# Optimization experiments

Measured on AMD Instinct MI355X. Metric: run time of the kernel, lower is better.

## Reference

```python
import jax, jax.numpy as jnp
import numpy as np

K = 3          # spline order
NUM = 32       # grid intervals G
IN_DIM = 256
OUT_DIM = 512
BATCH = 2048


def _b_spline_basis(x, grid, k):
    """Cox-de-Boor recursion. x: (B, I); grid: (I, G+2k+1) -> (B, I, G+k)."""
    xg = x[:, :, None]                      # (B, I, 1)
    g = grid[None, :, :]                    # (1, I, G+2k+1)
    val = ((xg >= g[:, :, :-1]) & (xg < g[:, :, 1:])).astype(x.dtype)
    for p in range(1, k + 1):
        left = (xg - g[:, :, :-(p + 1)]) / (g[:, :, p:-1] - g[:, :, :-(p + 1)])
        right = (g[:, :, p + 1:] - xg) / (g[:, :, p + 1:] - g[:, :, 1:-p])
        val = left * val[:, :, :-1] + right * val[:, :, 1:]
    return val                               # (B, I, G+k)


def setup_inputs() -> dict:
    key = jax.random.key(0)
    k1, k2, k3 = jax.random.split(key, 3)
    x = jax.random.normal(k1, (BATCH, IN_DIM), dtype=jnp.float32)
    # uniform grid on [-1, 1], extended by k knots on each side (extend_grid)
    base = np.linspace(-1.0, 1.0, NUM + 1)
    h = 2.0 / NUM
    ext = np.concatenate([base[0] - h * np.arange(K, 0, -1), base,
                          base[-1] + h * np.arange(1, K + 1)]).astype(np.float32)
    grid = jnp.tile(jnp.asarray(ext)[None, :], (IN_DIM, 1))  # (I, G+2k+1)
    coef = 0.1 * jax.random.normal(k2, (IN_DIM, OUT_DIM, NUM + K), dtype=jnp.float32)
    scale_base = jax.random.normal(k3, (IN_DIM, OUT_DIM), dtype=jnp.float32) / np.sqrt(IN_DIM).astype(np.float32)
    scale_sp = jnp.ones((IN_DIM, OUT_DIM), dtype=jnp.float32) / np.sqrt(IN_DIM).astype(np.float32)
    mask = jnp.ones((IN_DIM, OUT_DIM), dtype=jnp.float32)
    return {"x": x, "grid": grid, "coef": coef,
            "scale_base": scale_base, "scale_sp": scale_sp, "mask": mask}


def reference(x, grid, coef, scale_base, scale_sp, mask):
    base = jax.nn.silu(x)                                   # b(x) residual, (B, I)
    bases = _b_spline_basis(x, grid, K)                     # (B, I, G+k)
    # coef2curve: einsum('ijk,jlk->ijl') in pykan -> (B, I, O)
    y = jnp.einsum('bik,iok->bio', bases, coef)
    y = scale_base[None, :, :] * base[:, :, None] + scale_sp[None, :, :] * y
    y = mask[None, :, :] * y
    return jnp.sum(y, axis=1)                               # (B, O)
```

## Files before the change

kernel.cpp:

```cpp
#include <hip/hip_runtime.h>
#include <math.h>

#define BATCH   2048
#define IN_DIM  256
#define OUT_DIM 512
#define NK      35
#define KS      48
#define KG      6
#define BTILE   128
#define OTILE   128
#define ICHUNK  32
#define NSPLIT  8
#define NBUF    4
#define COEFS_BYTES ((size_t)IN_DIM * OUT_DIM * KS * 2)
#define PART_ELEMS  ((size_t)BATCH * OUT_DIM)

__device__ __forceinline__ unsigned short f2bf(float x) {
    unsigned u = __float_as_uint(x);
    u += 0x7FFF + ((u >> 16) & 1);
    return (unsigned short)(u >> 16);
}
__device__ __forceinline__ float bf2f(unsigned short h) {
    return __uint_as_float(((unsigned)h) << 16);
}
__device__ __forceinline__ unsigned pack2(unsigned short a, unsigned short b) {
    return (unsigned)a | ((unsigned)b << 16);
}

typedef __bf16 bf16x8 __attribute__((ext_vector_type(8)));
typedef float  f32x16 __attribute__((ext_vector_type(16)));
typedef int    i32x4  __attribute__((ext_vector_type(4)));
typedef unsigned int u32;

__device__ __forceinline__ void gload_lds16(const void* g, void* l) {
    __builtin_amdgcn_global_load_lds((const __attribute__((address_space(1))) u32*)g,
                                     (__attribute__((address_space(3))) u32*)l, 16, 0, 0);
}

__device__ __forceinline__ unsigned lds_off(const void* p) {
    return (unsigned)(uintptr_t)(const __attribute__((address_space(3))) char*)p;
}

__device__ __forceinline__ i32x4 ds_read128(unsigned base, int off) {
    i32x4 r;
    asm volatile("ds_read_b128 %0, %1 offset:%c2"
                 : "=v"(r) : "v"(base), "i"(off));
    return r;
}
__device__ __forceinline__ bf16x8 as_bf16x8(i32x4 v) {
    bf16x8 r; __builtin_memcpy(&r, &v, 16); return r;
}

#define PR 32
__global__ __launch_bounds__(256) void kan_prep(
    const float* __restrict__ coef,
    const float* __restrict__ scale_base,
    const float* __restrict__ scale_sp,
    const float* __restrict__ mask,
    unsigned short* __restrict__ coefS)
{
    __shared__ float sc[PR * NK];
    __shared__ float sspm[PR], ssbm[PR];
    const int t    = threadIdx.x;
    const int row0 = blockIdx.x * PR;

    {
        const float4* csrc = (const float4*)(coef + (size_t)row0 * NK);
        float4* cdst = (float4*)sc;
        cdst[t] = csrc[t];
        if (t < 24) cdst[t + 256] = csrc[t + 256];
    }
    if (t < PR) {
        float m = mask[row0 + t];
        sspm[t] = scale_sp[row0 + t] * m;
        ssbm[t] = scale_base[row0 + t] * m;
    }
    __syncthreads();

    if (t < PR * 6) {
        int r = t / 6;
        int q = t - r * 6;
        float spm = sspm[r];
        const float* c = sc + r * NK;
        uint4 v = make_uint4(0u, 0u, 0u, 0u);
        if (q < 4) {
            const float* cq = c + q * 8;
            v.x = pack2(f2bf(cq[0] * spm), f2bf(cq[1] * spm));
            v.y = pack2(f2bf(cq[2] * spm), f2bf(cq[3] * spm));
            v.z = pack2(f2bf(cq[4] * spm), f2bf(cq[5] * spm));
            v.w = pack2(f2bf(cq[6] * spm), f2bf(cq[7] * spm));
        } else if (q == 4) {
            float sbm = ssbm[r];
            unsigned short hi = f2bf(sbm);
            unsigned short lo = f2bf(sbm - bf2f(hi));
            v.x = pack2(f2bf(c[32] * spm), f2bf(c[33] * spm));
            v.y = pack2(f2bf(c[34] * spm), 0);
            v.z = pack2(hi, hi);
            v.w = pack2(lo, 0);
        }
        int g = row0 + r;
        size_t di = ((size_t)(((g >> 9) * 4 + ((g >> 7) & 3)) * 6 + q)) * 128
                  + (size_t)(g & 127);
        ((uint4*)coefS)[di] = v;
    }
}

__global__ __launch_bounds__(256, 2) void kan_mfma(
    const float* __restrict__ x,
    const unsigned short* __restrict__ coefS,
    float* __restrict__ part)
{
    __shared__ __align__(16) short sA[2 * BTILE * KS];
    __shared__ __align__(16) short sB[NBUF * OTILE * KS];

    const int t    = threadIdx.x;
    const int w    = t >> 6;
    const int lane = t & 63;
    const int l31  = lane & 31, lh = lane >> 5;
    const int wr   = w & 1;
    const int wc   = w >> 1;
    const int o0   = blockIdx.x * OTILE;
    const int b0   = blockIdx.y * BTILE;
    const int ic0  = blockIdx.z * ICHUNK;
    const bool bTh = (t >= 128);
    const int wbase = t & 64;

    {
        uint4 z = make_uint4(0, 0, 0, 0);
        #pragma unroll
        for (int u = 0; u < 6; ++u) {
            int idx = t + 256 * u;
            if (idx < (2 * BTILE * KS * 2) / 16) ((uint4*)sA)[idx] = z;
        }
    }

    f32x16 acc00 = {}, acc01 = {}, acc10 = {}, acc11 = {};

    float xreg = 0.0f;
    int ojb0 = 0, ojb1 = 0;

    auto stageA = [&](short* abuf, int row, float xv, int& ojbn) {
        #pragma unroll
        for (int qq = 0; qq < 4; ++qq) {
            int k = ojbn + qq;
            abuf[((k >> 3) * BTILE + row) * 8 + (k & 7)] = 0;
        }
        float xn = (xv + 1.1875f) * 16.0f;
        float jf = floorf(xn);
        int   j  = (int)jf;
        float u  = xn - jf;
        bool valid = (xn >= 0.0f) && (j <= 37);
        float u2 = u * u, u3 = u2 * u;
        float w0 = (1.0f / 6.0f) * (1.0f - 3.0f * u + 3.0f * u2 - u3);
        float w1 = (1.0f / 6.0f) * (3.0f * u3 - 6.0f * u2 + 4.0f);
        float w2 = (1.0f / 6.0f) * (-3.0f * u3 + 3.0f * u2 + 3.0f * u + 1.0f);
        float w3 = (1.0f / 6.0f) * u3;
        int jb = j - 3;
        if (valid) {
            if ((unsigned)jb < 35u) {
                int k = jb;     abuf[((k >> 3) * BTILE + row) * 8 + (k & 7)] = f2bf(w0);
            }
            if ((unsigned)(jb + 1) < 35u) {
                int k = jb + 1; abuf[((k >> 3) * BTILE + row) * 8 + (k & 7)] = f2bf(w1);
            }
            if ((unsigned)(jb + 2) < 35u) {
                int k = jb + 2; abuf[((k >> 3) * BTILE + row) * 8 + (k & 7)] = f2bf(w2);
            }
            if ((unsigned)(jb + 3) < 35u) {
                int k = jb + 3; abuf[((k >> 3) * BTILE + row) * 8 + (k & 7)] = f2bf(w3);
            }
        }
        ojbn = min(max(jb, 0), 31);
        float sig = 1.0f / (1.0f + __expf(-xv));
        float s   = xv * sig;
        unsigned short shi = f2bf(s);
        unsigned short slo = f2bf(s - bf2f(shi));
        short* k4 = abuf + (4 * BTILE + row) * 8;
        *(unsigned int*)(k4 + 4) = pack2(shi, slo);
        k4[6] = shi;
    };

    auto issueB = [&](int i, int buf) {
        const char* gsrc = (const char*)coefS
                         + ((size_t)i * 4 + (o0 >> 7)) * (KG * OTILE * 8 * 2);
        #pragma unroll
        for (int q = 0; q < 6; ++q) {
            int slot = wbase + (t & 63) + 128 * q;
            gload_lds16(gsrc + slot * 16,
                        (void*)(sB + buf * (OTILE * KS) + (wbase + 128 * q) * 8));
        }
    };

    __syncthreads();

    if (!bTh) {
        float x0 = x[(size_t)(b0 + t) * IN_DIM + ic0];
        stageA(sA, t, x0, ojb0);
        xreg = x[(size_t)(b0 + t) * IN_DIM + ic0 + 1];
    } else {
        issueB(ic0,     0);
        issueB(ic0 + 1, 1);
        issueB(ic0 + 2, 2);
    }
    if (bTh) asm volatile("s_waitcnt vmcnt(12)" ::: "memory");
    else     asm volatile("s_waitcnt lgkmcnt(0)" ::: "memory");
    __builtin_amdgcn_s_barrier();
    __builtin_amdgcn_sched_barrier(0);

    const unsigned sAoff = lds_off(sA);
    const unsigned sBoff = lds_off(sB);

    auto body = [&](int it, int& ojbn) {
        if (bTh && it + 1 < ICHUNK) {
            int ip3 = (it + 3 < ICHUNK) ? (it + 3) : (ICHUNK - 1);
            issueB(ic0 + ip3, (it + 3) & (NBUF - 1));
        }

        const int cur = it & 1;
        const unsigned Abo = sAoff
            + (unsigned)(cur * (BTILE * KS) + (lh * BTILE + wr * 64 + l31) * 8) * 2u;
        const unsigned Bbo = sBoff
            + (unsigned)((it & (NBUF - 1)) * (OTILE * KS)
                         + (lh * OTILE + wc * 64 + l31) * 8) * 2u;

        i32x4 a0r[3], a1r[3], b0r[3], b1r[3];
        #pragma unroll
        for (int s = 0; s < 3; ++s) {
            a0r[s] = ds_read128(Abo, s * 4096);
            a1r[s] = ds_read128(Abo, s * 4096 + 512);
            b0r[s] = ds_read128(Bbo, s * 4096);
            b1r[s] = ds_read128(Bbo, s * 4096 + 512);
        }
        asm volatile("s_waitcnt lgkmcnt(0)" ::: "memory");
        __builtin_amdgcn_sched_barrier(0);

        __builtin_amdgcn_s_setprio(1);
        #pragma unroll
        for (int s = 0; s < 3; ++s) {
            acc00 = __builtin_amdgcn_mfma_f32_32x32x16_bf16(as_bf16x8(a0r[s]), as_bf16x8(b0r[s]), acc00, 0, 0, 0);
            acc01 = __builtin_amdgcn_mfma_f32_32x32x16_bf16(as_bf16x8(a0r[s]), as_bf16x8(b1r[s]), acc01, 0, 0, 0);
            acc10 = __builtin_amdgcn_mfma_f32_32x32x16_bf16(as_bf16x8(a1r[s]), as_bf16x8(b0r[s]), acc10, 0, 0, 0);
            acc11 = __builtin_amdgcn_mfma_f32_32x32x16_bf16(as_bf16x8(a1r[s]), as_bf16x8(b1r[s]), acc11, 0, 0, 0);
        }
        __builtin_amdgcn_s_setprio(0);

        if (!bTh && it + 1 < ICHUNK) {
            stageA(sA + (cur ^ 1) * (BTILE * KS), t, xreg, ojbn);
            if (it + 2 < ICHUNK)
                xreg = x[(size_t)(b0 + t) * IN_DIM + ic0 + it + 2];
        }

        if (it + 1 < ICHUNK) {
            if (bTh) asm volatile("s_waitcnt vmcnt(12)" ::: "memory");
            else     asm volatile("s_waitcnt lgkmcnt(0)" ::: "memory");
            __builtin_amdgcn_s_barrier();
            __builtin_amdgcn_sched_barrier(0);
        }
    };

    for (int itp = 0; itp < ICHUNK / 2; ++itp) {
        body(2 * itp,     ojb1);
        body(2 * itp + 1, ojb0);
    }

    __syncthreads();

    float* tp = (float*)sA + w * (32 * 36);
    float* pdst = part + (size_t)blockIdx.z * PART_ELEMS;
    #pragma unroll
    for (int r = 0; r < 2; ++r) {
        #pragma unroll
        for (int c = 0; c < 2; ++c) {
            const f32x16& acc = (r == 0) ? ((c == 0) ? acc00 : acc01)
                                         : ((c == 0) ? acc10 : acc11);
            #pragma unroll
            for (int reg = 0; reg < 16; ++reg) {
                int row = (reg & 3) + 8 * (reg >> 2) + 4 * lh;
                tp[row * 36 + l31] = acc[reg];
            }
            int cc = (lane & 7) * 4;
            #pragma unroll
            for (int j = 0; j < 4; ++j) {
                int rr = j * 8 + (lane >> 3);
                float4 v = *(float4*)&tp[rr * 36 + cc];
                int rowg = b0 + wr * 64 + r * 32 + rr;
                int colg = o0 + wc * 64 + c * 32 + cc;
                *(float4*)&pdst[(size_t)rowg * OUT_DIM + colg] = v;
            }
        }
    }
}

__global__ __launch_bounds__(256) void kan_reduce(
    const float4* __restrict__ part, float4* __restrict__ out)
{
    const size_t e = (size_t)blockIdx.x * 256 + threadIdx.x;
    float4 s = part[e];
    #pragma unroll
    for (int z = 1; z < NSPLIT; ++z) {
        float4 v = part[(size_t)z * (PART_ELEMS / 4) + e];
        s.x += v.x; s.y += v.y; s.z += v.z; s.w += v.w;
    }
    out[e] = s;
}

extern "C" void kernel_launch(void* const* d_in, const int* in_sizes, int n_in,
                              void* d_out, int out_size, void* d_ws, size_t ws_size,
                              hipStream_t stream) {
    const float* x          = (const float*)d_in[0];
    const float* coef       = (const float*)d_in[2];
    const float* scale_base = (const float*)d_in[3];
    const float* scale_sp   = (const float*)d_in[4];
    const float* mask       = (const float*)d_in[5];
    unsigned short* coefS   = (unsigned short*)d_ws;
    float* part             = (float*)((char*)d_ws + COEFS_BYTES);

    kan_prep<<<dim3(IN_DIM * OUT_DIM / PR), dim3(256), 0, stream>>>(
        coef, scale_base, scale_sp, mask, coefS);
    kan_mfma<<<dim3(OUT_DIM / OTILE, BATCH / BTILE, NSPLIT), dim3(256), 0, stream>>>(
        x, coefS, part);
    kan_reduce<<<dim3(BATCH * OUT_DIM / 4 / 256), dim3(256), 0, stream>>>(
        (const float4*)part, (float4*)d_out);
}
```

Baseline: 120.3 us.

## Split input dim finer, double-buffer coef tiles, pack A-staging writes as 32-bit

Halves the per-block input chunk and doubles the split count, so there are twice as many blocks. The coefficient LDS ring shrinks from four buffers to two, which lowers LDS use enough to raise occupancy to three blocks per CU. The spline-weight staging now writes packed 32-bit pairs instead of individual 16-bit stores, and it is moved before the MFMA wait so its ALU and LDS work overlaps the fragment reads. The risks are a shallower prefetch (now only one tile ahead, with a full vmcnt(0) wait each step) and twice as many fp32 partial outputs to reduce.

```diff
diff --git a/kernel.cpp b/kernel.cpp
--- a/kernel.cpp
+++ b/kernel.cpp
@@ -9,9 +9,9 @@
 #define KG      6
 #define BTILE   128
 #define OTILE   128
-#define ICHUNK  32
-#define NSPLIT  8
-#define NBUF    4
+#define ICHUNK  16
+#define NSPLIT  16
+#define NBUF    2
 #define COEFS_BYTES ((size_t)IN_DIM * OUT_DIM * KS * 2)
 #define PART_ELEMS  ((size_t)BATCH * OUT_DIM)
 
@@ -105,7 +105,7 @@
     }
 }
 
-__global__ __launch_bounds__(256, 2) void kan_mfma(
+__global__ __launch_bounds__(256, 3) void kan_mfma(
     const float* __restrict__ x,
     const unsigned short* __restrict__ coefS,
     float* __restrict__ part)
@@ -137,14 +137,18 @@
     f32x16 acc00 = {}, acc01 = {}, acc10 = {}, acc11 = {};
 
     float xreg = 0.0f;
-    int ojb0 = 0, ojb1 = 0;
-
-    auto stageA = [&](short* abuf, int row, float xv, int& ojbn) {
-        #pragma unroll
-        for (int qq = 0; qq < 4; ++qq) {
-            int k = ojbn + qq;
-            abuf[((k >> 3) * BTILE + row) * 8 + (k & 7)] = 0;
-        }
+    int om0 = 0, om1 = 0;
+
+    auto stageA = [&](short* abuf, int row, float xv, int& omn) {
+        unsigned* rp = (unsigned*)abuf + row * 4;
+        auto PADDR = [&](int p) -> unsigned* {
+            return rp + (p >> 2) * (BTILE * 4) + (p & 3);
+        };
+        int oc = omn;
+        *PADDR(oc)     = 0;
+        *PADDR(oc + 1) = 0;
+        *PADDR(oc + 2) = 0;
+
         float xn = (xv + 1.1875f) * 16.0f;
         float jf = floorf(xn);
         int   j  = (int)jf;
@@ -156,28 +160,26 @@
         float w2 = (1.0f / 6.0f) * (-3.0f * u3 + 3.0f * u2 + 3.0f * u + 1.0f);
         float w3 = (1.0f / 6.0f) * u3;
         int jb = j - 3;
+        unsigned short h0 = f2bf(w0), h1 = f2bf(w1), h2 = f2bf(w2), h3 = f2bf(w3);
+        int  m0  = jb >> 1;
+        bool odd = (jb & 1) != 0;
+        unsigned C0 = odd ? pack2(0, h0)
+                          : (jb == 34 ? pack2(h0, 0) : pack2(h0, h1));
+        unsigned C1 = odd ? (jb == 33 ? pack2(h1, 0) : pack2(h1, h2))
+                          : (jb == 32 ? pack2(h2, 0) : pack2(h2, h3));
+        unsigned C2 = pack2(h3, 0);
         if (valid) {
-            if ((unsigned)jb < 35u) {
-                int k = jb;     abuf[((k >> 3) * BTILE + row) * 8 + (k & 7)] = f2bf(w0);
-            }
-            if ((unsigned)(jb + 1) < 35u) {
-                int k = jb + 1; abuf[((k >> 3) * BTILE + row) * 8 + (k & 7)] = f2bf(w1);
-            }
-            if ((unsigned)(jb + 2) < 35u) {
-                int k = jb + 2; abuf[((k >> 3) * BTILE + row) * 8 + (k & 7)] = f2bf(w2);
-            }
-            if ((unsigned)(jb + 3) < 35u) {
-                int k = jb + 3; abuf[((k >> 3) * BTILE + row) * 8 + (k & 7)] = f2bf(w3);
-            }
-        }
-        ojbn = min(max(jb, 0), 31);
+            if (m0 >= 0)                        *PADDR(m0)     = C0;
+            if (m0 + 1 >= 0 && jb != 34)        *PADDR(m0 + 1) = C1;
+            if (odd && jb != 33 && m0 + 2 >= 0) *PADDR(m0 + 2) = C2;
+        }
+        omn = min(max(m0, 0), 15);
         float sig = 1.0f / (1.0f + __expf(-xv));
         float s   = xv * sig;
         unsigned short shi = f2bf(s);
         unsigned short slo = f2bf(s - bf2f(shi));
-        short* k4 = abuf + (4 * BTILE + row) * 8;
-        *(unsigned int*)(k4 + 4) = pack2(shi, slo);
-        k4[6] = shi;
+        uint2 bw; bw.x = pack2(shi, slo); bw.y = pack2(shi, 0);
+        *(uint2*)PADDR(18) = bw;
     };
 
     auto issueB = [&](int i, int buf) {
@@ -195,14 +197,12 @@
 
     if (!bTh) {
         float x0 = x[(size_t)(b0 + t) * IN_DIM + ic0];
-        stageA(sA, t, x0, ojb0);
+        stageA(sA, t, x0, om0);
         xreg = x[(size_t)(b0 + t) * IN_DIM + ic0 + 1];
     } else {
-        issueB(ic0,     0);
-        issueB(ic0 + 1, 1);
-        issueB(ic0 + 2, 2);
-    }
-    if (bTh) asm volatile("s_waitcnt vmcnt(12)" ::: "memory");
+        issueB(ic0, 0);
+    }
+    if (bTh) asm volatile("s_waitcnt vmcnt(0)" ::: "memory");
     else     asm volatile("s_waitcnt lgkmcnt(0)" ::: "memory");
     __builtin_amdgcn_s_barrier();
     __builtin_amdgcn_sched_barrier(0);
@@ -210,18 +210,14 @@
     const unsigned sAoff = lds_off(sA);
     const unsigned sBoff = lds_off(sB);
 
-    auto body = [&](int it, int& ojbn) {
-        if (bTh && it + 1 < ICHUNK) {
-            int ip3 = (it + 3 < ICHUNK) ? (it + 3) : (ICHUNK - 1);
-            issueB(ic0 + ip3, (it + 3) & (NBUF - 1));
-        }
+    auto body = [&](int it, int& omn) {
+        if (bTh && it + 1 < ICHUNK) issueB(ic0 + it + 1, (it + 1) & 1);
 
         const int cur = it & 1;
         const unsigned Abo = sAoff
             + (unsigned)(cur * (BTILE * KS) + (lh * BTILE + wr * 64 + l31) * 8) * 2u;
         const unsigned Bbo = sBoff
-            + (unsigned)((it & (NBUF - 1)) * (OTILE * KS)
-                         + (lh * OTILE + wc * 64 + l31) * 8) * 2u;
+            + (unsigned)(cur * (OTILE * KS) + (lh * OTILE + wc * 64 + l31) * 8) * 2u;
 
         i32x4 a0r[3], a1r[3], b0r[3], b1r[3];
         #pragma unroll
@@ -231,6 +227,13 @@
             b0r[s] = ds_read128(Bbo, s * 4096);
             b1r[s] = ds_read128(Bbo, s * 4096 + 512);
         }
+
+        if (!bTh && it + 1 < ICHUNK) {
+            stageA(sA + ((it + 1) & 1) * (BTILE * KS), t, xreg, omn);
+            if (it + 2 < ICHUNK)
+                xreg = x[(size_t)(b0 + t) * IN_DIM + ic0 + it + 2];
+        }
+
         asm volatile("s_waitcnt lgkmcnt(0)" ::: "memory");
         __builtin_amdgcn_sched_barrier(0);
 
@@ -244,23 +247,16 @@
         }
         __builtin_amdgcn_s_setprio(0);
 
-        if (!bTh && it + 1 < ICHUNK) {
-            stageA(sA + (cur ^ 1) * (BTILE * KS), t, xreg, ojbn);
-            if (it + 2 < ICHUNK)
-                xreg = x[(size_t)(b0 + t) * IN_DIM + ic0 + it + 2];
-        }
-
         if (it + 1 < ICHUNK) {
-            if (bTh) asm volatile("s_waitcnt vmcnt(12)" ::: "memory");
-            else     asm volatile("s_waitcnt lgkmcnt(0)" ::: "memory");
+            if (bTh) asm volatile("s_waitcnt vmcnt(0)" ::: "memory");
             __builtin_amdgcn_s_barrier();
             __builtin_amdgcn_sched_barrier(0);
         }
     };
 
     for (int itp = 0; itp < ICHUNK / 2; ++itp) {
-        body(2 * itp,     ojb1);
-        body(2 * itp + 1, ojb0);
+        body(2 * itp,     om1);
+        body(2 * itp + 1, om0);
     }
 
     __syncthreads();
```

New measurement: 131.3 us. 9.1% more time.
